# Kernel optimization log

Measured on AMD Instinct MI355X. Metric: run time of the kernel, lower is better.

## Reference

```python
import jax, jax.numpy as jnp
import numpy as np


def setup_inputs() -> dict:
    key = jax.random.key(0)
    k1, k2, k3, k4 = jax.random.split(key, 4)
    B, H, L, D = 2, 16, 2048, 64
    q = jax.random.normal(k1, (B, H, L, D), dtype=jnp.float32)
    k = jax.random.normal(k2, (B, H, L, D), dtype=jnp.float32)
    v = jax.random.normal(k3, (B, H, L, D), dtype=jnp.float32)
    mask = jax.random.randint(k4, (B, 1, L, L), 0, 2, dtype=jnp.int32)
    return {"q": q, "k": k, "v": v, "mask": mask}


def reference(q, k, v, mask):
    d_tensor = q.shape[-1]
    # NegativeReLU: pass through only negative values and 0
    v_neg = -jax.nn.relu(-v)
    # score: [B,H,L,L]
    score = jnp.einsum("bhqd,bhkd->bhqk", q, k) / jnp.sqrt(
        jnp.asarray(d_tensor, dtype=q.dtype))
    score = jnp.where(mask == 0, jnp.asarray(-10000.0, dtype=score.dtype), score)
    attn = jax.nn.softmax(score, axis=-1)
    return jnp.einsum("bhqk,bhkd->bhqd", attn, v_neg)
```

## Files before the change

### kernel.cpp

```cpp
#include <hip/hip_runtime.h>
#include <math.h>

typedef __bf16 bf16_t;
typedef bf16_t bf16x8 __attribute__((ext_vector_type(8)));
typedef float  f32x16 __attribute__((ext_vector_type(16)));
typedef float  f32x4  __attribute__((ext_vector_type(4)));

#define MFMA32(a, b, c) __builtin_amdgcn_mfma_f32_32x32x16_bf16((a), (b), (c), 0, 0, 0)

static __device__ __forceinline__ unsigned pk_bf16(float a, float b) {
  union { bf16_t h[2]; unsigned u; } t;
  t.h[0] = (bf16_t)a;
  t.h[1] = (bf16_t)b;
  return t.u;
}

static __device__ __forceinline__ unsigned pk_trunc(float a, float b) {
  return (__float_as_uint(a) >> 16) | (__float_as_uint(b) & 0xFFFF0000u);
}

__global__ __launch_bounds__(256) void prepass(
    const float* __restrict__ kp, const float* __restrict__ vp,
    const int* __restrict__ maskp, bf16_t* __restrict__ kfr,
    bf16_t* __restrict__ vfr, unsigned long long* __restrict__ mpk) {
  const int sect = blockIdx.x >> 11;
  const int blk  = blockIdx.x & 2047;
  const int tid  = threadIdx.x;

  if (sect == 0) {
    const size_t t = (size_t)blk * 256 + tid;
    const int ln = t & 63, dc = (t >> 6) & 3;
    const int kh = (t >> 8) & 63, bh = (int)(t >> 14);
    const float* s = kp + ((size_t)(bh * 2048 + kh * 32 + (ln & 31))) * 64 +
                     dc * 16 + (ln >> 5) * 8;
    f32x4 a0 = *(const f32x4*)s;
    f32x4 a1 = *(const f32x4*)(s + 4);
    bf16x8 w;
#pragma unroll
    for (int j = 0; j < 4; ++j) { w[j] = (bf16_t)a0[j]; w[4 + j] = (bf16_t)a1[j]; }
    *(bf16x8*)(kfr + t * 8) = w;
  } else if (sect == 1) {
    const size_t t = (size_t)blk * 256 + tid;
    const int ln = t & 63, rr = (t >> 6) & 1, kc = (t >> 7) & 1;
    const int p = (t >> 8) & 1, kt = (t >> 9) & 31, bh = (int)(t >> 14);
    const int d    = rr * 32 + (ln & 31);
    const int hh   = ln >> 5;
    const int kb   = kt * 64 + p * 32 + kc * 16;
    const float* s = vp + ((size_t)(bh * 2048 + kb)) * 64 + d;
    bf16_t w[8];
#pragma unroll
    for (int j = 0; j < 8; ++j) {
      const int key = hh * 4 + (j & 3) + 8 * (j >> 2);
      w[j] = (bf16_t)fminf(s[(size_t)key * 64], 0.f);
    }
    *(bf16x8*)(vfr + t * 8) = *(bf16x8*)w;
  } else {
    const int lane = tid & 63;
    const int gw   = blk * 4 + (tid >> 6);
    const int bq   = gw >> 1, half = gw & 1;
    const int b    = bq >> 11, q = bq & 2047;
    const size_t base = (size_t)bq * 2048 + half * 1024;
    unsigned long long w = 0;
#pragma unroll
    for (int j = 0; j < 16; ++j) {
      const int mv = maskp[base + j * 64 + lane];
      const unsigned long long bal = __ballot(mv != 0);
      if (lane == j) w = bal;
    }
    if (lane < 16) mpk[((size_t)b * 32 + half * 16 + lane) * 2048 + q] = w;
  }
}

__global__ __launch_bounds__(256, 4) void nrev_attn_ws(
    const float* __restrict__ qp, const bf16_t* __restrict__ kfr,
    const bf16_t* __restrict__ vfr, const unsigned long long* __restrict__ mpk,
    float* __restrict__ outp) {
  constexpr int L = 2048, D = 64;
  __shared__ float Oe[2][64][68];
  __shared__ float lsum[2][2][2][32];

  const int tid  = threadIdx.x;
  const int lane = tid & 63;
  const int wv   = tid >> 6;
  const int p    = wv >> 1;
  const int g    = wv & 1;
  const int col  = lane & 31;
  const int hh   = lane >> 5;
  const int blk  = blockIdx.x;
  const int bh   = (blk & 7) * 4 + (blk >> 8);
  const int qt   = (blk >> 3) & 31;
  const int bb   = bh >> 4;
  const int q0   = qt * 64;
  const float c1 = 0.18033688011112042f;

  bf16x8 qf[4];
  {
    const float* gq = qp + (size_t)(bh * L + q0 + g * 32 + col) * D;
#pragma unroll
    for (int dc = 0; dc < 4; ++dc) {
      const float* ptr = gq + dc * 16 + hh * 8;
      f32x4 f0 = *(const f32x4*)ptr;
      f32x4 f1 = *(const f32x4*)(ptr + 4);
      bf16x8 t;
#pragma unroll
      for (int j = 0; j < 4; ++j) {
        t[j]     = (bf16_t)(f0[j] * c1);
        t[4 + j] = (bf16_t)(f1[j] * c1);
      }
      qf[dc] = t;
    }
  }

  const char* kpt = (const char*)kfr + (size_t)bh * 262144 + p * 4096 + (size_t)lane * 16;
  const char* vpt = (const char*)vfr + (size_t)bh * 262144 + p * 4096 + (size_t)lane * 16;
  const unsigned long long* mrow = mpk + (size_t)bb * 65536 + q0 + g * 32 + col;

  f32x16 acc0, acc1;
#pragma unroll
  for (int i = 0; i < 16; ++i) { acc0[i] = 0.f; acc1[i] = 0.f; }
  float l_run = 0.f;

  bf16x8 kf0 = *(const bf16x8*)(kpt + 0);
  bf16x8 kf1 = *(const bf16x8*)(kpt + 1024);
  bf16x8 kf2 = *(const bf16x8*)(kpt + 2048);
  bf16x8 kf3 = *(const bf16x8*)(kpt + 3072);
  unsigned long long bits = mrow[0];

  for (int it = 0; it < 32; ++it) {
    const int itn = (it < 31) ? it + 1 : 31;
    const char* kn = kpt + (size_t)itn * 8192;
    bf16x8 kn0 = *(const bf16x8*)(kn + 0);
    bf16x8 kn1 = *(const bf16x8*)(kn + 1024);
    bf16x8 kn2 = *(const bf16x8*)(kn + 2048);
    bf16x8 kn3 = *(const bf16x8*)(kn + 3072);
    const char* vg = vpt + (size_t)it * 8192;
    bf16x8 vf0 = *(const bf16x8*)(vg + 0);
    bf16x8 vf1 = *(const bf16x8*)(vg + 1024);
    bf16x8 vf2 = *(const bf16x8*)(vg + 2048);
    bf16x8 vf3 = *(const bf16x8*)(vg + 3072);
    const unsigned long long bits_n = mrow[(size_t)itn * 2048];

    f32x16 st0;
#pragma unroll
    for (int i = 0; i < 16; ++i) st0[i] = 0.f;
    st0 = MFMA32(kf0, qf[0], st0);
    st0 = MFMA32(kf1, qf[1], st0);
    st0 = MFMA32(kf2, qf[2], st0);
    st0 = MFMA32(kf3, qf[3], st0);

    const unsigned kb32 = ((unsigned)(bits >> (32 * p))) >> (4 * hh);
    float Sl = 0.f;
#pragma unroll
    for (int r = 0; r < 16; ++r) {
      const int c = (r & 3) + 8 * (r >> 2);
      float p0 = __builtin_amdgcn_exp2f(st0[r]);
      p0 = ((kb32 >> c) & 1u) ? p0 : 0.f;
      st0[r] = p0;
      Sl += p0;
    }
    l_run += Sl;

#pragma unroll
    for (int kc = 0; kc < 2; ++kc) {
      union { unsigned u[4]; bf16x8 v; } bbv;
      bbv.u[0] = pk_trunc(st0[8 * kc + 0], st0[8 * kc + 1]);
      bbv.u[1] = pk_trunc(st0[8 * kc + 2], st0[8 * kc + 3]);
      bbv.u[2] = pk_trunc(st0[8 * kc + 4], st0[8 * kc + 5]);
      bbv.u[3] = pk_trunc(st0[8 * kc + 6], st0[8 * kc + 7]);
      if (kc == 0) {
        acc0 = MFMA32(vf0, bbv.v, acc0);
        acc1 = MFMA32(vf1, bbv.v, acc1);
      } else {
        acc0 = MFMA32(vf2, bbv.v, acc0);
        acc1 = MFMA32(vf3, bbv.v, acc1);
      }
    }

    kf0 = kn0; kf1 = kn1; kf2 = kn2; kf3 = kn3;
    bits = bits_n;
  }

  lsum[g][p][hh][col] = l_run;
  __syncthreads();
  const float scale = 1.f / (lsum[g][0][0][col] + lsum[g][0][1][col] +
                             lsum[g][1][0][col] + lsum[g][1][1][col]);

#pragma unroll
  for (int dt = 0; dt < 2; ++dt)
#pragma unroll
    for (int g2 = 0; g2 < 4; ++g2) {
      f32x4 w;
#pragma unroll
      for (int j = 0; j < 4; ++j)
        w[j] = (dt ? acc1[g2 * 4 + j] : acc0[g2 * 4 + j]) * scale;
      *(f32x4*)&Oe[p][g * 32 + col][g2 * 8 + hh * 4 + dt * 32] = w;
    }
  __syncthreads();
#pragma unroll
  for (int i = 0; i < 4; ++i) {
    const int idx = tid + i * 256;
    const int row = idx >> 4, c4 = idx & 15;
    f32x4 v0 = *(const f32x4*)&Oe[0][row][c4 * 4];
    f32x4 v1 = *(const f32x4*)&Oe[1][row][c4 * 4];
    f32x4 vs = v0 + v1;
    *(f32x4*)&outp[(size_t)(bh * L + q0 + row) * D + c4 * 4] = vs;
  }
}

__global__ __launch_bounds__(256, 4) void nrev_attn_fb(
    const float* __restrict__ qp, const float* __restrict__ kp,
    const float* __restrict__ vp, const int* __restrict__ maskp,
    float* __restrict__ outp) {
  constexpr int L = 2048, D = 64;
  __shared__ union alignas(16) SMem {
    struct {
      bf16_t K[64 * 72];
      bf16_t V[64 * 72];
      unsigned long long mb[64];
    } s;
    float Oe[2][64][68];
  } sm;
  __shared__ float mlbuf[2][2][32][2];

  const int tid  = threadIdx.x;
  const int lane = tid & 63;
  const int wv   = tid >> 6;
  const int p    = wv >> 1;
  const int g    = wv & 1;
  const int col  = lane & 31;
  const int hh   = lane >> 5;
  const int blk  = blockIdx.x;
  const int bh   = (blk & 7) * 4 + (blk >> 8);
  const int qt   = (blk >> 3) & 31;
  const int bb   = bh >> 4;
  const int q0   = qt * 64;
  const float c1 = 0.18033688011112042f;

  bf16x8 qf[4];
  {
    const float* gq = qp + (size_t)(bh * L + q0 + g * 32 + col) * D;
#pragma unroll
    for (int dc = 0; dc < 4; ++dc) {
      const float* ptr = gq + dc * 16 + hh * 8;
      f32x4 f0 = *(const f32x4*)ptr;
      f32x4 f1 = *(const f32x4*)(ptr + 4);
      bf16x8 t;
#pragma unroll
      for (int j = 0; j < 4; ++j) {
        t[j]     = (bf16_t)(f0[j] * c1);
        t[4 + j] = (bf16_t)(f1[j] * c1);
      }
      qf[dc] = t;
    }
  }

  f32x16 acc0, acc1;
#pragma unroll
  for (int i = 0; i < 16; ++i) { acc0[i] = 0.f; acc1[i] = 0.f; }
  float m_run = -__builtin_inff();
  float l_run = 0.f;

  for (int kt = 0; kt < L; kt += 64) {
    __syncthreads();
    {
      const int key = tid >> 2, dp = tid & 3;
      const float* gk = kp + (size_t)(bh * L + kt + key) * D + dp * 16;
      f32x4 a0 = *(const f32x4*)gk;
      f32x4 a1 = *(const f32x4*)(gk + 4);
      f32x4 a2 = *(const f32x4*)(gk + 8);
      f32x4 a3 = *(const f32x4*)(gk + 12);
      bf16x8 w0, w1;
#pragma unroll
      for (int j = 0; j < 4; ++j) {
        w0[j] = (bf16_t)a0[j]; w0[4 + j] = (bf16_t)a1[j];
        w1[j] = (bf16_t)a2[j]; w1[4 + j] = (bf16_t)a3[j];
      }
      *(bf16x8*)&sm.s.K[key * 72 + dp * 16]     = w0;
      *(bf16x8*)&sm.s.K[key * 72 + dp * 16 + 8] = w1;
    }
    {
      const int w16 = wv * 16;
      const float* gv = vp + (size_t)(bh * L + kt + w16) * D + lane;
      bf16x8 w0, w1;
#pragma unroll
      for (int i = 0; i < 8; ++i) {
        w0[i] = (bf16_t)fminf(gv[(size_t)i * D], 0.f);
        w1[i] = (bf16_t)fminf(gv[(size_t)(i + 8) * D], 0.f);
      }
      *(bf16x8*)&sm.s.V[lane * 72 + w16]     = w0;
      *(bf16x8*)&sm.s.V[lane * 72 + w16 + 8] = w1;
    }
    for (int i = 0; i < 16; ++i) {
      const int row = wv * 16 + i;
      int mv = maskp[(size_t)bb * L * L + (size_t)(q0 + row) * L + kt + lane];
      unsigned long long bal = __ballot(mv != 0);
      if (lane == 0) sm.s.mb[row] = bal;
    }
    __syncthreads();

    f32x16 st0;
#pragma unroll
    for (int i = 0; i < 16; ++i) st0[i] = 0.f;
#pragma unroll
    for (int dc = 0; dc < 4; ++dc) {
      bf16x8 a0 = *(const bf16x8*)&sm.s.K[(p * 32 + col) * 72 + dc * 16 + hh * 8];
      st0 = MFMA32(a0, qf[dc], st0);
    }

    float M = st0[0];
#pragma unroll
    for (int r = 1; r < 16; ++r) M = fmaxf(M, st0[r]);
#pragma unroll
    for (int sh = 1; sh < 64; sh <<= 1) M = fmaxf(M, __shfl_xor(M, sh));
    if (M > m_run) {
      const float alpha = exp2f(m_run - M);
      l_run *= alpha;
#pragma unroll
      for (int r = 0; r < 16; ++r) { acc0[r] *= alpha; acc1[r] *= alpha; }
      m_run = M;
    }

    const unsigned long long bits = sm.s.mb[g * 32 + col];
    const unsigned kb = ((unsigned)(bits >> (32 * p))) >> (4 * hh);
    float Sl = 0.f;
#pragma unroll
    for (int r = 0; r < 16; ++r) {
      const int c = (r & 3) + 8 * (r >> 2);
      float p0 = exp2f(st0[r] - m_run);
      p0 = ((kb >> c) & 1u) ? p0 : 0.f;
      st0[r] = p0;
      Sl += p0;
    }
    Sl += __shfl_xor(Sl, 32);
    l_run += Sl;

#pragma unroll
    for (int kc = 0; kc < 2; ++kc) {
      const unsigned pk0  = pk_bf16(st0[8 * kc + 0], st0[8 * kc + 1]);
      const unsigned pk0b = pk_bf16(st0[8 * kc + 2], st0[8 * kc + 3]);
      const unsigned pk1  = pk_bf16(st0[8 * kc + 4], st0[8 * kc + 5]);
      const unsigned pk1b = pk_bf16(st0[8 * kc + 6], st0[8 * kc + 7]);
      const unsigned sh0  = __shfl_xor(pk0, 32);
      const unsigned sh0b = __shfl_xor(pk0b, 32);
      const unsigned sh1  = __shfl_xor(pk1, 32);
      const unsigned sh1b = __shfl_xor(pk1b, 32);
      union { unsigned u[4]; bf16x8 v; } bbv;
      bbv.u[0] = hh ? sh1  : pk0;
      bbv.u[1] = hh ? sh1b : pk0b;
      bbv.u[2] = hh ? pk1  : sh0;
      bbv.u[3] = hh ? pk1b : sh0b;
      const int kbase = p * 32 + kc * 16 + hh * 8;
      bf16x8 av0 = *(const bf16x8*)&sm.s.V[col * 72        + kbase];
      bf16x8 av1 = *(const bf16x8*)&sm.s.V[(col + 32) * 72 + kbase];
      acc0 = MFMA32(av0, bbv.v, acc0);
      acc1 = MFMA32(av1, bbv.v, acc1);
    }
  }

  if (hh == 0) {
    mlbuf[g][p][col][0] = m_run;
    mlbuf[g][p][col][1] = l_run;
  }
  __syncthreads();
  const float m0 = mlbuf[g][0][col][0], l0v = mlbuf[g][0][col][1];
  const float m1 = mlbuf[g][1][col][0], l1v = mlbuf[g][1][col][1];
  const float ms = fmaxf(m0, m1);
  const float a0s = exp2f(m0 - ms), a1s = exp2f(m1 - ms);
  const float lst = a0s * l0v + a1s * l1v;
  const float scale = (p ? a1s : a0s) / lst;

#pragma unroll
  for (int dt = 0; dt < 2; ++dt)
#pragma unroll
    for (int g2 = 0; g2 < 4; ++g2) {
      f32x4 w;
#pragma unroll
      for (int j = 0; j < 4; ++j)
        w[j] = (dt ? acc1[g2 * 4 + j] : acc0[g2 * 4 + j]) * scale;
      *(f32x4*)&sm.Oe[p][g * 32 + col][g2 * 8 + hh * 4 + dt * 32] = w;
    }
  __syncthreads();
#pragma unroll
  for (int i = 0; i < 4; ++i) {
    const int idx = tid + i * 256;
    const int row = idx >> 4, c4 = idx & 15;
    f32x4 v0 = *(const f32x4*)&sm.Oe[0][row][c4 * 4];
    f32x4 v1 = *(const f32x4*)&sm.Oe[1][row][c4 * 4];
    f32x4 vs = v0 + v1;
    *(f32x4*)&outp[(size_t)(bh * L + q0 + row) * D + c4 * 4] = vs;
  }
}

extern "C" void kernel_launch(void* const* d_in, const int* in_sizes, int n_in,
                              void* d_out, int out_size, void* d_ws, size_t ws_size,
                              hipStream_t stream) {
  (void)in_sizes; (void)n_in; (void)out_size;
  const float* qp = (const float*)d_in[0];
  const float* kp = (const float*)d_in[1];
  const float* vp = (const float*)d_in[2];
  const int*   mp = (const int*)d_in[3];
  float* op = (float*)d_out;

  const size_t kOff = 0;
  const size_t vOff = (size_t)8 * 1024 * 1024;
  const size_t mOff = (size_t)16 * 1024 * 1024;
  const size_t need = mOff + (size_t)1024 * 1024;

  if (d_ws != nullptr && ws_size >= need) {
    bf16_t* kb = (bf16_t*)((char*)d_ws + kOff);
    bf16_t* vt = (bf16_t*)((char*)d_ws + vOff);
    unsigned long long* mpk = (unsigned long long*)((char*)d_ws + mOff);
    hipLaunchKernelGGL(prepass, dim3(6144), dim3(256), 0, stream,
                       kp, vp, mp, kb, vt, mpk);
    hipLaunchKernelGGL(nrev_attn_ws, dim3(1024), dim3(256), 0, stream,
                       qp, kb, vt, mpk, op);
  } else {
    hipLaunchKernelGGL(nrev_attn_fb, dim3(1024), dim3(256), 0, stream,
                       qp, kp, vp, mp, op);
  }
}
```

Before: 160.6 us.

## Expand mask to bf16 bitmasks and drop online softmax max tracking

Adds a new prepass that expands the int32 mask into 16-bit AND-masks laid out to match the MFMA fragments, plus a new attention kernel that skips the running max. It exponentiates scores directly with exp2 and masks them by bitwise AND, and accumulates the row sum through an MFMA against a vector of ones. The aim is to remove the per-tile max/rescale work and the mask-decoding ALU from the inner loop. In exchange it needs a larger workspace, and it relies on scores staying within exp2 range, which holds for these random normal inputs but is not a general safe softmax.

```diff
diff --git a/kernel.cpp b/kernel.cpp
--- a/kernel.cpp
+++ b/kernel.cpp
@@ -17,6 +17,199 @@
 
 static __device__ __forceinline__ unsigned pk_trunc(float a, float b) {
   return (__float_as_uint(a) >> 16) | (__float_as_uint(b) & 0xFFFF0000u);
+}
+
+__global__ __launch_bounds__(256) void prepass2(
+    const float* __restrict__ kp, const float* __restrict__ vp,
+    const int* __restrict__ maskp, bf16_t* __restrict__ kfr,
+    bf16_t* __restrict__ vfr, unsigned* __restrict__ mw) {
+  const int bx  = blockIdx.x;
+  const int tid = threadIdx.x;
+
+  if (bx < 2048) {
+    const size_t t = (size_t)bx * 256 + tid;
+    const int ln = t & 63, dc = (t >> 6) & 3;
+    const int kh = (t >> 8) & 63, bh = (int)(t >> 14);
+    const float* s = kp + ((size_t)(bh * 2048 + kh * 32 + (ln & 31))) * 64 +
+                     dc * 16 + (ln >> 5) * 8;
+    f32x4 a0 = *(const f32x4*)s;
+    f32x4 a1 = *(const f32x4*)(s + 4);
+    bf16x8 w;
+#pragma unroll
+    for (int j = 0; j < 4; ++j) { w[j] = (bf16_t)a0[j]; w[4 + j] = (bf16_t)a1[j]; }
+    *(bf16x8*)(kfr + t * 8) = w;
+  } else if (bx < 4096) {
+    const size_t t = (size_t)(bx - 2048) * 256 + tid;
+    const int ln = t & 63, rr = (t >> 6) & 1, kc = (t >> 7) & 1;
+    const int p = (t >> 8) & 1, kt = (t >> 9) & 31, bh = (int)(t >> 14);
+    const int d    = rr * 32 + (ln & 31);
+    const int hh   = ln >> 5;
+    const int kb   = kt * 64 + p * 32 + kc * 16;
+    const float* s = vp + ((size_t)(bh * 2048 + kb)) * 64 + d;
+    bf16_t w[8];
+#pragma unroll
+    for (int j = 0; j < 8; ++j) {
+      const int key = hh * 4 + (j & 3) + 8 * (j >> 2);
+      w[j] = (bf16_t)fminf(s[(size_t)key * 64], 0.f);
+    }
+    *(bf16x8*)(vfr + t * 8) = *(bf16x8*)w;
+  } else {
+    const unsigned gt = (unsigned)(bx - 4096) * 256u + (unsigned)tid;
+    const int hh = gt & 1;
+    const int q  = (gt >> 1) & 2047;
+    const int kc = (gt >> 12) & 1;
+    const int p  = (gt >> 13) & 1;
+    const int kt = (gt >> 14) & 31;
+    const int b  = (int)(gt >> 19);
+    const int kb = kt * 64 + p * 32 + kc * 16 + hh * 4;
+    const int* mr = maskp + ((size_t)b * 2048 + q) * 2048 + kb;
+    const int4 a = *(const int4*)mr;
+    const int4 c = *(const int4*)(mr + 8);
+    uint4 w;
+    w.x = (a.x ? 0xFFFFu : 0u) | (a.y ? 0xFFFF0000u : 0u);
+    w.y = (a.z ? 0xFFFFu : 0u) | (a.w ? 0xFFFF0000u : 0u);
+    w.z = (c.x ? 0xFFFFu : 0u) | (c.y ? 0xFFFF0000u : 0u);
+    w.w = (c.z ? 0xFFFFu : 0u) | (c.w ? 0xFFFF0000u : 0u);
+    const size_t widx =
+        ((size_t)(b * 128 + kt * 4 + p * 2 + kc) * 2048 + q) * 8 + hh * 4;
+    *(uint4*)(mw + widx) = w;
+  }
+}
+
+__global__ __launch_bounds__(256, 3) void nrev_attn_ws2(
+    const float* __restrict__ qp, const bf16_t* __restrict__ kfr,
+    const bf16_t* __restrict__ vfr, const unsigned* __restrict__ mw,
+    float* __restrict__ outp) {
+  constexpr int L = 2048, D = 64;
+  __shared__ float Oe[2][64][68];
+  __shared__ float lsum[2][2][32];
+
+  const int tid  = threadIdx.x;
+  const int lane = tid & 63;
+  const int wv   = tid >> 6;
+  const int p    = wv >> 1;
+  const int g    = wv & 1;
+  const int col  = lane & 31;
+  const int hh   = lane >> 5;
+  const int blk  = blockIdx.x;
+  const int bh   = (blk & 7) * 4 + (blk >> 8);
+  const int qt   = (blk >> 3) & 31;
+  const int bb   = bh >> 4;
+  const int q0   = qt * 64;
+  const float c1 = 0.18033688011112042f;
+
+  bf16x8 qf[4];
+  {
+    const float* gq = qp + (size_t)(bh * L + q0 + g * 32 + col) * D;
+#pragma unroll
+    for (int dc = 0; dc < 4; ++dc) {
+      const float* ptr = gq + dc * 16 + hh * 8;
+      f32x4 f0 = *(const f32x4*)ptr;
+      f32x4 f1 = *(const f32x4*)(ptr + 4);
+      bf16x8 t;
+#pragma unroll
+      for (int j = 0; j < 4; ++j) {
+        t[j]     = (bf16_t)(f0[j] * c1);
+        t[4 + j] = (bf16_t)(f1[j] * c1);
+      }
+      qf[dc] = t;
+    }
+  }
+
+  const char* kpt = (const char*)kfr + (size_t)bh * 262144 + p * 4096 + (size_t)lane * 16;
+  const char* vpt = (const char*)vfr + (size_t)bh * 262144 + p * 4096 + (size_t)lane * 16;
+  const int   qq  = q0 + g * 32 + col;
+  const char* mpt = (const char*)mw +
+                    ((size_t)(bb * 128 + p * 2) * 2048 + qq) * 32 + hh * 16;
+
+  union { unsigned u[4]; bf16x8 v; } onesu;
+  onesu.u[0] = onesu.u[1] = onesu.u[2] = onesu.u[3] = 0x3F803F80u;
+  const bf16x8 onesv = onesu.v;
+
+  f32x16 acc0, acc1, accL;
+#pragma unroll
+  for (int i = 0; i < 16; ++i) { acc0[i] = 0.f; acc1[i] = 0.f; accL[i] = 0.f; }
+
+  bf16x8 kf0 = *(const bf16x8*)(kpt + 0);
+  bf16x8 kf1 = *(const bf16x8*)(kpt + 1024);
+  bf16x8 kf2 = *(const bf16x8*)(kpt + 2048);
+  bf16x8 kf3 = *(const bf16x8*)(kpt + 3072);
+  uint4 mc0 = *(const uint4*)(mpt);
+  uint4 mc1 = *(const uint4*)(mpt + 65536);
+
+  for (int it = 0; it < 32; ++it) {
+    const int itn = (it < 31) ? it + 1 : 31;
+    const char* kn = kpt + (size_t)itn * 8192;
+    bf16x8 kn0 = *(const bf16x8*)(kn + 0);
+    bf16x8 kn1 = *(const bf16x8*)(kn + 1024);
+    bf16x8 kn2 = *(const bf16x8*)(kn + 2048);
+    bf16x8 kn3 = *(const bf16x8*)(kn + 3072);
+    const char* mn = mpt + (size_t)itn * 262144;
+    uint4 mn0 = *(const uint4*)(mn);
+    uint4 mn1 = *(const uint4*)(mn + 65536);
+    const char* vg = vpt + (size_t)it * 8192;
+    bf16x8 vf0 = *(const bf16x8*)(vg + 0);
+    bf16x8 vf1 = *(const bf16x8*)(vg + 1024);
+    bf16x8 vf2 = *(const bf16x8*)(vg + 2048);
+    bf16x8 vf3 = *(const bf16x8*)(vg + 3072);
+
+    f32x16 st0;
+#pragma unroll
+    for (int i = 0; i < 16; ++i) st0[i] = 0.f;
+    st0 = MFMA32(kf0, qf[0], st0);
+    st0 = MFMA32(kf1, qf[1], st0);
+    st0 = MFMA32(kf2, qf[2], st0);
+    st0 = MFMA32(kf3, qf[3], st0);
+
+#pragma unroll
+    for (int r = 0; r < 16; ++r) st0[r] = __builtin_amdgcn_exp2f(st0[r]);
+
+    union { unsigned u[4]; bf16x8 v; } b0;
+    b0.u[0] = pk_bf16(st0[0], st0[1]) & mc0.x;
+    b0.u[1] = pk_bf16(st0[2], st0[3]) & mc0.y;
+    b0.u[2] = pk_bf16(st0[4], st0[5]) & mc0.z;
+    b0.u[3] = pk_bf16(st0[6], st0[7]) & mc0.w;
+    acc0 = MFMA32(vf0, b0.v, acc0);
+    acc1 = MFMA32(vf1, b0.v, acc1);
+    accL = MFMA32(onesv, b0.v, accL);
+
+    union { unsigned u[4]; bf16x8 v; } b1;
+    b1.u[0] = pk_bf16(st0[8],  st0[9])  & mc1.x;
+    b1.u[1] = pk_bf16(st0[10], st0[11]) & mc1.y;
+    b1.u[2] = pk_bf16(st0[12], st0[13]) & mc1.z;
+    b1.u[3] = pk_bf16(st0[14], st0[15]) & mc1.w;
+    acc0 = MFMA32(vf2, b1.v, acc0);
+    acc1 = MFMA32(vf3, b1.v, acc1);
+    accL = MFMA32(onesv, b1.v, accL);
+
+    kf0 = kn0; kf1 = kn1; kf2 = kn2; kf3 = kn3;
+    mc0 = mn0; mc1 = mn1;
+  }
+
+  if (hh == 0) lsum[g][p][col] = accL[0];
+  __syncthreads();
+  const float scale = 1.f / (lsum[g][0][col] + lsum[g][1][col]);
+
+#pragma unroll
+  for (int dt = 0; dt < 2; ++dt)
+#pragma unroll
+    for (int g2 = 0; g2 < 4; ++g2) {
+      f32x4 w;
+#pragma unroll
+      for (int j = 0; j < 4; ++j)
+        w[j] = (dt ? acc1[g2 * 4 + j] : acc0[g2 * 4 + j]) * scale;
+      *(f32x4*)&Oe[p][g * 32 + col][g2 * 8 + hh * 4 + dt * 32] = w;
+    }
+  __syncthreads();
+#pragma unroll
+  for (int i = 0; i < 4; ++i) {
+    const int idx = tid + i * 256;
+    const int row = idx >> 4, c4 = idx & 15;
+    f32x4 v0 = *(const f32x4*)&Oe[0][row][c4 * 4];
+    f32x4 v1 = *(const f32x4*)&Oe[1][row][c4 * 4];
+    f32x4 vs = v0 + v1;
+    *(f32x4*)&outp[(size_t)(bh * L + q0 + row) * D + c4 * 4] = vs;
+  }
 }
 
 __global__ __launch_bounds__(256) void prepass(
@@ -401,12 +594,21 @@
   const int*   mp = (const int*)d_in[3];
   float* op = (float*)d_out;
 
-  const size_t kOff = 0;
-  const size_t vOff = (size_t)8 * 1024 * 1024;
-  const size_t mOff = (size_t)16 * 1024 * 1024;
-  const size_t need = mOff + (size_t)1024 * 1024;
-
-  if (d_ws != nullptr && ws_size >= need) {
+  const size_t kOff  = 0;
+  const size_t vOff  = (size_t)8 * 1024 * 1024;
+  const size_t mOff  = (size_t)16 * 1024 * 1024;
+  const size_t need2 = (size_t)32 * 1024 * 1024;
+  const size_t need1 = mOff + (size_t)1024 * 1024;
+
+  if (d_ws != nullptr && ws_size >= need2) {
+    bf16_t* kb = (bf16_t*)((char*)d_ws + kOff);
+    bf16_t* vt = (bf16_t*)((char*)d_ws + vOff);
+    unsigned* mwp = (unsigned*)((char*)d_ws + mOff);
+    hipLaunchKernelGGL(prepass2, dim3(8192), dim3(256), 0, stream,
+                       kp, vp, mp, kb, vt, mwp);
+    hipLaunchKernelGGL(nrev_attn_ws2, dim3(1024), dim3(256), 0, stream,
+                       qp, kb, vt, mwp, op);
+  } else if (d_ws != nullptr && ws_size >= need1) {
     bf16_t* kb = (bf16_t*)((char*)d_ws + kOff);
     bf16_t* vt = (bf16_t*)((char*)d_ws + vOff);
     unsigned long long* mpk = (unsigned long long*)((char*)d_ws + mOff);
```

Measured after the change: 173.4 us. 1.08x slower.

## Fold mask into MFMA bias init and compute row sums via ones-MFMA

Applied to the files above, without the earlier changes.

Mask words are repacked in the prepass into per-lane 32-bit words in MFMA register order. Masked positions are then applied as a large negative initial accumulator value, so exp2 underflows to zero and the per-element select after exp disappears. The softmax denominator is accumulated by an extra MFMA against a ones vector instead of scalar adds, and probabilities are now rounded to bf16 rather than truncated. This trades VALU work for extra matrix instructions and a different mask prepass that loads the int mask with wide per-thread loads.

```diff
diff --git a/kernel.cpp b/kernel.cpp
--- a/kernel.cpp
+++ b/kernel.cpp
@@ -15,20 +15,23 @@
   return t.u;
 }
 
-static __device__ __forceinline__ unsigned pk_trunc(float a, float b) {
-  return (__float_as_uint(a) >> 16) | (__float_as_uint(b) & 0xFFFF0000u);
-}
-
-__global__ __launch_bounds__(256) void prepass(
+static __device__ __forceinline__ int bit_smear(unsigned w, int pos) {
+#if __has_builtin(__builtin_amdgcn_sbfe)
+  return __builtin_amdgcn_sbfe((int)w, pos, 1);
+#else
+  return ((int)(w << (31 - pos))) >> 31;
+#endif
+}
+
+__global__ __launch_bounds__(256) void prepass3(
     const float* __restrict__ kp, const float* __restrict__ vp,
     const int* __restrict__ maskp, bf16_t* __restrict__ kfr,
-    bf16_t* __restrict__ vfr, unsigned long long* __restrict__ mpk) {
-  const int sect = blockIdx.x >> 11;
-  const int blk  = blockIdx.x & 2047;
-  const int tid  = threadIdx.x;
-
-  if (sect == 0) {
-    const size_t t = (size_t)blk * 256 + tid;
+    bf16_t* __restrict__ vfr, unsigned* __restrict__ mq) {
+  const int bx  = blockIdx.x;
+  const int tid = threadIdx.x;
+
+  if (bx < 2048) {
+    const size_t t = (size_t)bx * 256 + tid;
     const int ln = t & 63, dc = (t >> 6) & 3;
     const int kh = (t >> 8) & 63, bh = (int)(t >> 14);
     const float* s = kp + ((size_t)(bh * 2048 + kh * 32 + (ln & 31))) * 64 +
@@ -39,8 +42,8 @@
 #pragma unroll
     for (int j = 0; j < 4; ++j) { w[j] = (bf16_t)a0[j]; w[4 + j] = (bf16_t)a1[j]; }
     *(bf16x8*)(kfr + t * 8) = w;
-  } else if (sect == 1) {
-    const size_t t = (size_t)blk * 256 + tid;
+  } else if (bx < 4096) {
+    const size_t t = (size_t)(bx - 2048) * 256 + tid;
     const int ln = t & 63, rr = (t >> 6) & 1, kc = (t >> 7) & 1;
     const int p = (t >> 8) & 1, kt = (t >> 9) & 31, bh = (int)(t >> 14);
     const int d    = rr * 32 + (ln & 31);
@@ -55,29 +58,36 @@
     }
     *(bf16x8*)(vfr + t * 8) = *(bf16x8*)w;
   } else {
-    const int lane = tid & 63;
-    const int gw   = blk * 4 + (tid >> 6);
-    const int bq   = gw >> 1, half = gw & 1;
-    const int b    = bq >> 11, q = bq & 2047;
-    const size_t base = (size_t)bq * 2048 + half * 1024;
-    unsigned long long w = 0;
-#pragma unroll
-    for (int j = 0; j < 16; ++j) {
-      const int mv = maskp[base + j * 64 + lane];
-      const unsigned long long bal = __ballot(mv != 0);
-      if (lane == j) w = bal;
-    }
-    if (lane < 16) mpk[((size_t)b * 32 + half * 16 + lane) * 2048 + q] = w;
-  }
-}
-
-__global__ __launch_bounds__(256, 4) void nrev_attn_ws(
+    const unsigned gt = (unsigned)(bx - 4096) * 256u + (unsigned)tid;
+    const int q  = gt & 2047;
+    const int p  = (gt >> 11) & 1;
+    const int it = (gt >> 12) & 31;
+    const int b  = (int)(gt >> 17);
+    const int* mr = maskp + ((size_t)b * 2048 + q) * 2048 + it * 64 + p * 32;
+    int m[32];
+#pragma unroll
+    for (int i = 0; i < 8; ++i) {
+      const int4 a = *(const int4*)(mr + i * 4);
+      m[i * 4 + 0] = a.x; m[i * 4 + 1] = a.y;
+      m[i * 4 + 2] = a.z; m[i * 4 + 3] = a.w;
+    }
+    unsigned w = 0;
+#pragma unroll
+    for (int j = 0; j < 32; ++j) {
+      const int koff = (j & 3) + 8 * ((j >> 2) & 3) + 4 * (j >> 4);
+      if (m[koff] == 0) w |= (1u << j);
+    }
+    mq[((size_t)(b * 32 + it) * 2 + p) * 2048 + q] = w;
+  }
+}
+
+__global__ __launch_bounds__(256, 4) void nrev_attn_ws3(
     const float* __restrict__ qp, const bf16_t* __restrict__ kfr,
-    const bf16_t* __restrict__ vfr, const unsigned long long* __restrict__ mpk,
+    const bf16_t* __restrict__ vfr, const unsigned* __restrict__ mq,
     float* __restrict__ outp) {
   constexpr int L = 2048, D = 64;
   __shared__ float Oe[2][64][68];
-  __shared__ float lsum[2][2][2][32];
+  __shared__ float lsum[2][2][32];
 
   const int tid  = threadIdx.x;
   const int lane = tid & 63;
@@ -86,6 +96,7 @@
   const int g    = wv & 1;
   const int col  = lane & 31;
   const int hh   = lane >> 5;
+  const int hsh  = hh << 4;
   const int blk  = blockIdx.x;
   const int bh   = (blk & 7) * 4 + (blk >> 8);
   const int qt   = (blk >> 3) & 31;
@@ -113,18 +124,22 @@
 
   const char* kpt = (const char*)kfr + (size_t)bh * 262144 + p * 4096 + (size_t)lane * 16;
   const char* vpt = (const char*)vfr + (size_t)bh * 262144 + p * 4096 + (size_t)lane * 16;
-  const unsigned long long* mrow = mpk + (size_t)bb * 65536 + q0 + g * 32 + col;
-
-  f32x16 acc0, acc1;
-#pragma unroll
-  for (int i = 0; i < 16; ++i) { acc0[i] = 0.f; acc1[i] = 0.f; }
-  float l_run = 0.f;
+  const int   qq  = q0 + g * 32 + col;
+  const unsigned* mpt = mq + ((size_t)bb * 64 + p) * 2048 + qq;
+
+  union { unsigned u[4]; bf16x8 v; } onesu;
+  onesu.u[0] = onesu.u[1] = onesu.u[2] = onesu.u[3] = 0x3F803F80u;
+  const bf16x8 onesv = onesu.v;
+
+  f32x16 acc0, acc1, accL;
+#pragma unroll
+  for (int i = 0; i < 16; ++i) { acc0[i] = 0.f; acc1[i] = 0.f; accL[i] = 0.f; }
 
   bf16x8 kf0 = *(const bf16x8*)(kpt + 0);
   bf16x8 kf1 = *(const bf16x8*)(kpt + 1024);
   bf16x8 kf2 = *(const bf16x8*)(kpt + 2048);
   bf16x8 kf3 = *(const bf16x8*)(kpt + 3072);
-  unsigned long long bits = mrow[0];
+  unsigned bitsw = mpt[0];
 
   for (int it = 0; it < 32; ++it) {
     const int itn = (it < 31) ? it + 1 : 31;
@@ -133,57 +148,52 @@
     bf16x8 kn1 = *(const bf16x8*)(kn + 1024);
     bf16x8 kn2 = *(const bf16x8*)(kn + 2048);
     bf16x8 kn3 = *(const bf16x8*)(kn + 3072);
+    const unsigned bw_n = mpt[(size_t)itn * 4096];
     const char* vg = vpt + (size_t)it * 8192;
     bf16x8 vf0 = *(const bf16x8*)(vg + 0);
     bf16x8 vf1 = *(const bf16x8*)(vg + 1024);
     bf16x8 vf2 = *(const bf16x8*)(vg + 2048);
     bf16x8 vf3 = *(const bf16x8*)(vg + 3072);
-    const unsigned long long bits_n = mrow[(size_t)itn * 2048];
-
+
+    const unsigned wsh = bitsw >> hsh;
     f32x16 st0;
 #pragma unroll
-    for (int i = 0; i < 16; ++i) st0[i] = 0.f;
+    for (int r = 0; r < 16; ++r)
+      st0[r] = __uint_as_float((unsigned)bit_smear(wsh, r) & 0xC6800000u);
+
     st0 = MFMA32(kf0, qf[0], st0);
     st0 = MFMA32(kf1, qf[1], st0);
     st0 = MFMA32(kf2, qf[2], st0);
     st0 = MFMA32(kf3, qf[3], st0);
 
-    const unsigned kb32 = ((unsigned)(bits >> (32 * p))) >> (4 * hh);
-    float Sl = 0.f;
-#pragma unroll
-    for (int r = 0; r < 16; ++r) {
-      const int c = (r & 3) + 8 * (r >> 2);
-      float p0 = __builtin_amdgcn_exp2f(st0[r]);
-      p0 = ((kb32 >> c) & 1u) ? p0 : 0.f;
-      st0[r] = p0;
-      Sl += p0;
-    }
-    l_run += Sl;
-
-#pragma unroll
-    for (int kc = 0; kc < 2; ++kc) {
-      union { unsigned u[4]; bf16x8 v; } bbv;
-      bbv.u[0] = pk_trunc(st0[8 * kc + 0], st0[8 * kc + 1]);
-      bbv.u[1] = pk_trunc(st0[8 * kc + 2], st0[8 * kc + 3]);
-      bbv.u[2] = pk_trunc(st0[8 * kc + 4], st0[8 * kc + 5]);
-      bbv.u[3] = pk_trunc(st0[8 * kc + 6], st0[8 * kc + 7]);
-      if (kc == 0) {
-        acc0 = MFMA32(vf0, bbv.v, acc0);
-        acc1 = MFMA32(vf1, bbv.v, acc1);
-      } else {
-        acc0 = MFMA32(vf2, bbv.v, acc0);
-        acc1 = MFMA32(vf3, bbv.v, acc1);
-      }
-    }
+#pragma unroll
+    for (int r = 0; r < 16; ++r) st0[r] = __builtin_amdgcn_exp2f(st0[r]);
+
+    union { unsigned u[4]; bf16x8 v; } b0;
+    b0.u[0] = pk_bf16(st0[0], st0[1]);
+    b0.u[1] = pk_bf16(st0[2], st0[3]);
+    b0.u[2] = pk_bf16(st0[4], st0[5]);
+    b0.u[3] = pk_bf16(st0[6], st0[7]);
+    acc0 = MFMA32(vf0, b0.v, acc0);
+    acc1 = MFMA32(vf1, b0.v, acc1);
+    accL = MFMA32(onesv, b0.v, accL);
+
+    union { unsigned u[4]; bf16x8 v; } b1;
+    b1.u[0] = pk_bf16(st0[8],  st0[9]);
+    b1.u[1] = pk_bf16(st0[10], st0[11]);
+    b1.u[2] = pk_bf16(st0[12], st0[13]);
+    b1.u[3] = pk_bf16(st0[14], st0[15]);
+    acc0 = MFMA32(vf2, b1.v, acc0);
+    acc1 = MFMA32(vf3, b1.v, acc1);
+    accL = MFMA32(onesv, b1.v, accL);
 
     kf0 = kn0; kf1 = kn1; kf2 = kn2; kf3 = kn3;
-    bits = bits_n;
-  }
-
-  lsum[g][p][hh][col] = l_run;
+    bitsw = bw_n;
+  }
+
+  if (hh == 0) lsum[g][p][col] = accL[0];
   __syncthreads();
-  const float scale = 1.f / (lsum[g][0][0][col] + lsum[g][0][1][col] +
-                             lsum[g][1][0][col] + lsum[g][1][1][col]);
+  const float scale = 1.f / (lsum[g][0][col] + lsum[g][1][col]);
 
 #pragma unroll
   for (int dt = 0; dt < 2; ++dt)
@@ -409,11 +419,11 @@
   if (d_ws != nullptr && ws_size >= need) {
     bf16_t* kb = (bf16_t*)((char*)d_ws + kOff);
     bf16_t* vt = (bf16_t*)((char*)d_ws + vOff);
-    unsigned long long* mpk = (unsigned long long*)((char*)d_ws + mOff);
-    hipLaunchKernelGGL(prepass, dim3(6144), dim3(256), 0, stream,
-                       kp, vp, mp, kb, vt, mpk);
-    hipLaunchKernelGGL(nrev_attn_ws, dim3(1024), dim3(256), 0, stream,
-                       qp, kb, vt, mpk, op);
+    unsigned* mqp = (unsigned*)((char*)d_ws + mOff);
+    hipLaunchKernelGGL(prepass3, dim3(5120), dim3(256), 0, stream,
+                       kp, vp, mp, kb, vt, mqp);
+    hipLaunchKernelGGL(nrev_attn_ws3, dim3(1024), dim3(256), 0, stream,
+                       qp, kb, vt, mqp, op);
   } else {
     hipLaunchKernelGGL(nrev_attn_fb, dim3(1024), dim3(256), 0, stream,
                        qp, kp, vp, mp, op);
```

Result: slower. 168.6 us (+5.0%).
